# Performance work log

Measured on AMD Instinct MI355X. Metric: run time of the kernel, lower is better.

## Reference

```python
import jax, jax.numpy as jnp
import numpy as np

B = 8
SEQ = 8192
D_MODEL = 256
D_STATE = 64
D_CONV = 4
EXPAND = 4
HEADDIM = 64
N_LAYERS = 8
D_INNER = EXPAND * D_MODEL            # 1024
NHEADS = D_INNER // HEADDIM           # 16
CONV_DIM = D_INNER + 2 * D_STATE      # 1152 (ngroups=1)
D_IN_PROJ = 2 * D_INNER + 2 * D_STATE + NHEADS  # 2192


def setup_inputs():
    key = jax.random.key(0)
    ks = jax.random.split(key, 16)
    rn = lambda k, shape, fan: jax.random.normal(k, shape, jnp.float32) / np.float32(np.sqrt(fan))
    inp = {}
    inp["x"] = jax.random.normal(ks[0], (B, 3, SEQ), jnp.float32)
    inp["conv1_w"] = rn(ks[1], (64, 3, 16), 3 * 16)
    inp["conv1_b"] = rn(ks[2], (64,), 64)
    inp["conv2_w"] = rn(ks[3], (D_MODEL, 64, 16), 64 * 16)
    inp["conv2_b"] = rn(ks[4], (D_MODEL,), D_MODEL)
    inp["in_proj_w"] = rn(ks[5], (N_LAYERS, D_IN_PROJ, D_MODEL), D_MODEL)
    inp["dw_conv_w"] = rn(ks[6], (N_LAYERS, CONV_DIM, D_CONV), D_CONV)
    inp["dw_conv_b"] = rn(ks[7], (N_LAYERS, CONV_DIM), D_CONV)
    inp["dt_bias"] = jax.random.normal(ks[8], (N_LAYERS, NHEADS), jnp.float32) * 0.5
    inp["A_log"] = jax.random.uniform(ks[9], (N_LAYERS, NHEADS), jnp.float32, 0.0, 2.0)
    inp["ssm_D"] = jnp.ones((N_LAYERS, NHEADS), jnp.float32)
    inp["rms_w"] = jnp.ones((N_LAYERS, D_INNER), jnp.float32)
    inp["out_proj_w"] = rn(ks[10], (N_LAYERS, D_MODEL, D_INNER), D_INNER)
    inp["ln_w"] = jnp.ones((D_MODEL,), jnp.float32)
    inp["ln_b"] = jnp.zeros((D_MODEL,), jnp.float32)
    inp["reg1_w"] = rn(ks[11], (128, D_MODEL), D_MODEL)
    inp["reg1_b"] = rn(ks[12], (128,), 128)
    inp["reg2_w"] = rn(ks[13], (1, 128), 128)
    inp["reg2_b"] = rn(ks[14], (1,), 128)
    return inp


def _silu(v):
    return v * jax.nn.sigmoid(v)


def _mamba2_layer(u, in_proj_w, dw_w, dw_b, dt_bias, A_log, ssm_D, rms_w, out_proj_w):
    b, l, _ = u.shape
    zxbcdt = u @ in_proj_w.T                               # (b,l,2192)
    z = zxbcdt[..., :D_INNER]
    xBC = zxbcdt[..., D_INNER:D_INNER + CONV_DIM]
    dt = jax.nn.softplus(zxbcdt[..., D_INNER + CONV_DIM:] + dt_bias)   # (b,l,h)
    # causal depthwise conv1d (kernel D_CONV), then SiLU
    pad = jnp.pad(xBC, ((0, 0), (D_CONV - 1, 0), (0, 0)))
    conv = sum(pad[:, k:k + l, :] * dw_w[:, k] for k in range(D_CONV)) + dw_b
    xBC = _silu(conv)
    xh = xBC[..., :D_INNER].reshape(b, l, NHEADS, HEADDIM)  # (b,l,h,p)
    Bm = xBC[..., D_INNER:D_INNER + D_STATE]                # (b,l,n)
    Cm = xBC[..., D_INNER + D_STATE:]                       # (b,l,n)
    dA = jnp.exp(dt * (-jnp.exp(A_log)))                    # (b,l,h)

    def step(h, inp):
        dA_t, dt_t, x_t, B_t, C_t = inp
        h = h * dA_t[:, :, None, None] + (dt_t[:, :, None] * x_t)[..., None] * B_t[:, None, None, :]
        y = jnp.einsum('bhpn,bn->bhp', h, C_t)
        return h, y

    h0 = jnp.zeros((b, NHEADS, HEADDIM, D_STATE), u.dtype)
    xs = (dA.transpose(1, 0, 2), dt.transpose(1, 0, 2),
          xh.transpose(1, 0, 2, 3), Bm.transpose(1, 0, 2), Cm.transpose(1, 0, 2))
    _, ys = jax.lax.scan(step, h0, xs)                      # (l,b,h,p)
    y = ys.transpose(1, 0, 2, 3) + ssm_D[None, None, :, None] * xh
    y = y.reshape(b, l, D_INNER)
    y = y * _silu(z)                                        # gated
    y = y * jax.lax.rsqrt(jnp.mean(y * y, axis=-1, keepdims=True) + 1e-5) * rms_w
    return y @ out_proj_w.T


def reference(x, conv1_w, conv1_b, conv2_w, conv2_b, in_proj_w, dw_conv_w, dw_conv_b,
              dt_bias, A_log, ssm_D, rms_w, out_proj_w, ln_w, ln_b,
              reg1_w, reg1_b, reg2_w, reg2_b):
    dn = ('NCH', 'OIH', 'NCH')
    h = jax.lax.conv_general_dilated(x, conv1_w, (4,), [(6, 6)], dimension_numbers=dn) + conv1_b[None, :, None]
    h = jax.nn.gelu(h, approximate=False)
    h = jax.lax.conv_general_dilated(h, conv2_w, (2,), [(7, 7)], dimension_numbers=dn) + conv2_b[None, :, None]
    h = jax.nn.gelu(h, approximate=False)
    h = h.transpose(0, 2, 1)                                # (b, 1024, d_model)
    for i in range(N_LAYERS):
        h = _mamba2_layer(h, in_proj_w[i], dw_conv_w[i], dw_conv_b[i],
                          dt_bias[i], A_log[i], ssm_D[i], rms_w[i], out_proj_w[i])
    mu = jnp.mean(h, -1, keepdims=True)
    var = jnp.mean((h - mu) ** 2, -1, keepdims=True)
    h = (h - mu) * jax.lax.rsqrt(var + 1e-5) * ln_w + ln_b  # LayerNorm
    pooled = h.mean(1)
    r = jax.nn.gelu(pooled @ reg1_w.T + reg1_b, approximate=False)
    return r @ reg2_w.T + reg2_b                            # (b, 1)
```

## Files before the change

kernel.cpp:

```cpp
#include <hip/hip_runtime.h>
#include <math.h>

#define NB       8
#define SEQ      8192
#define L1OUT    2048
#define LOUT     1024
#define DMODEL   256
#define DINNER   1024
#define NHEADS   16
#define HEADDIM  64
#define DSTATE   64
#define CONVDIM  1152
#define DINPROJ  2192
#define NPADIN   2304
#define NLAYERS  8
#define NCHUNK   16
#define Q        64

typedef _Float16 f16;
typedef __attribute__((ext_vector_type(8))) _Float16 f16x8;
typedef __attribute__((ext_vector_type(4))) _Float16 f16x4;
typedef __attribute__((ext_vector_type(4))) float    f32x4;

__device__ __forceinline__ float gelu_f(float v) {
    return 0.5f * v * (1.0f + erff(v * 0.70710678118654752f));
}
__device__ __forceinline__ float silu_f(float v) {
    return v * __builtin_amdgcn_rcpf(1.0f + __expf(-v));
}

__device__ __forceinline__ void gload16(const void* g, void* l) {
    __builtin_amdgcn_global_load_lds(
        (const __attribute__((address_space(1))) unsigned int*)g,
        (__attribute__((address_space(3))) unsigned int*)l, 16, 0, 0);
}

__global__ __launch_bounds__(256) void k_cast(const float* __restrict__ in,
                                              f16* __restrict__ out, int n) {
    int i = blockIdx.x * 256 + threadIdx.x;
    if (i < n) out[i] = (f16)in[i];
}

__global__ __launch_bounds__(256) void k_cast_inproj(const float* __restrict__ w,
                                                     f16* __restrict__ out) {
    int idx = blockIdx.x * 256 + threadIdx.x;
    int c = idx & 255;
    int r = (idx >> 8) % NPADIN;
    int l = idx / (NPADIN * 256);
    float v = (r < DINPROJ) ? w[((size_t)l * DINPROJ + r) * 256 + c] : 0.f;
    out[idx] = (f16)v;
}

__global__ __launch_bounds__(256) void k_conv1(const float* __restrict__ x,
                                               const float* __restrict__ w,
                                               const float* __restrict__ bias,
                                               f16* __restrict__ out) {
    int idx = blockIdx.x * 256 + threadIdx.x;
    int u  = idx & 255;
    int co = (idx >> 8) & 63;
    int b  = idx >> 14;
    int xbase = u * 32 - 8;

    float acc[8];
#pragma unroll
    for (int t = 0; t < 8; ++t) acc[t] = bias[co];

#pragma unroll
    for (int ci = 0; ci < 3; ++ci) {
        const float* xp = x + ((size_t)b * 3 + ci) * SEQ;
        float xb[48];
#pragma unroll
        for (int j = 0; j < 12; ++j) {
            int off = xbase + j * 4;
            float4 v;
            if (off >= 0 && off + 3 < SEQ) {
                v = *(const float4*)&xp[off];
            } else {
                v.x = (off + 0 >= 0 && off + 0 < SEQ) ? xp[off + 0] : 0.f;
                v.y = (off + 1 >= 0 && off + 1 < SEQ) ? xp[off + 1] : 0.f;
                v.z = (off + 2 >= 0 && off + 2 < SEQ) ? xp[off + 2] : 0.f;
                v.w = (off + 3 >= 0 && off + 3 < SEQ) ? xp[off + 3] : 0.f;
            }
            xb[j * 4 + 0] = v.x; xb[j * 4 + 1] = v.y;
            xb[j * 4 + 2] = v.z; xb[j * 4 + 3] = v.w;
        }
        const float* wp = w + (co * 3 + ci) * 16;
        float wv[16];
#pragma unroll
        for (int k = 0; k < 16; ++k) wv[k] = wp[k];
#pragma unroll
        for (int t = 0; t < 8; ++t)
#pragma unroll
            for (int k = 0; k < 16; ++k)
                acc[t] = fmaf(xb[t * 4 + k + 2], wv[k], acc[t]);
    }
    f16x8 o;
#pragma unroll
    for (int t = 0; t < 8; ++t) o[t] = (f16)gelu_f(acc[t]);
    *(f16x8*)&out[((size_t)(b * 64 + co)) * L1OUT + u * 8] = o;
}

__global__ __launch_bounds__(256) void k_im2col(const f16* __restrict__ h1,
                                                f16* __restrict__ A) {
    int idx = blockIdx.x * 256 + threadIdx.x;
    int g = idx & 127;
    int row = idx >> 7;
    int t = row & (LOUT - 1);
    int b = row >> 10;
    int ci = g >> 1, k0 = (g & 1) * 8;
    int pos0 = t * 2 + k0 - 7;
    const f16* hp = h1 + ((size_t)(b * 64 + ci)) * L1OUT;
    f16x8 v;
#pragma unroll
    for (int j = 0; j < 8; ++j) {
        int p = pos0 + j;
        v[j] = (p >= 0 && p < L1OUT) ? hp[p] : (f16)0.f;
    }
    *(f16x8*)&A[(size_t)row * 1024 + g * 8] = v;
}

template<int BM, int EPI>
__global__ __launch_bounds__(256) void k_hgemm(const f16* __restrict__ A,
                                               const f16* __restrict__ Bw,
                                               f16* __restrict__ Ch,
                                               int M, int N, int K,
                                               const float* __restrict__ bias,
                                               const float* __restrict__ dt_bias,
                                               const float* __restrict__ A_log,
                                               float* __restrict__ dadt) {
    constexpr int MI = BM / 32;
    __shared__ f16 As[BM * 64];
    __shared__ f16 Bs[128 * 64];
    int tid  = threadIdx.x;
    int lane = tid & 63, wid = tid >> 6;
    int wm = wid >> 1, wn = wid & 1;
    int row0 = blockIdx.y * BM, col0 = blockIdx.x * 128;
    int lr = lane & 15, kb = lane >> 4;

    f32x4 acc[MI][4];
#pragma unroll
    for (int mi = 0; mi < MI; ++mi)
#pragma unroll
        for (int ni = 0; ni < 4; ++ni)
            acc[mi][ni] = (f32x4){0.f, 0.f, 0.f, 0.f};

    int sr  = tid >> 3;
    int scx = ((tid & 7) ^ (sr & 7)) * 8;
    int rsw = (lr & 7) * 8;

    for (int k0 = 0; k0 < K; k0 += 64) {
        __syncthreads();
#pragma unroll
        for (int is = 0; is < BM / 32; ++is)
            gload16(A + (size_t)(row0 + is * 32 + sr) * K + k0 + scx,
                    &As[is * 2048 + wid * 512]);
#pragma unroll
        for (int is = 0; is < 4; ++is)
            gload16(Bw + (size_t)(col0 + is * 32 + sr) * K + k0 + scx,
                    &Bs[is * 2048 + wid * 512]);
        __syncthreads();

#pragma unroll
        for (int ks = 0; ks < 2; ++ks) {
            int cbase = (ks * 32 + kb * 8) ^ rsw;
            f16x8 a[MI], b[4];
#pragma unroll
            for (int mi = 0; mi < MI; ++mi)
                a[mi] = *reinterpret_cast<const f16x8*>(
                    &As[(wm * (BM / 2) + mi * 16 + lr) * 64 + cbase]);
#pragma unroll
            for (int ni = 0; ni < 4; ++ni)
                b[ni] = *reinterpret_cast<const f16x8*>(
                    &Bs[(wn * 64 + ni * 16 + lr) * 64 + cbase]);
#pragma unroll
            for (int mi = 0; mi < MI; ++mi)
#pragma unroll
                for (int ni = 0; ni < 4; ++ni)
                    acc[mi][ni] = __builtin_amdgcn_mfma_f32_16x16x32_f16(
                        a[mi], b[ni], acc[mi][ni], 0, 0, 0);
        }
    }

#pragma unroll
    for (int mi = 0; mi < MI; ++mi)
#pragma unroll
        for (int ni = 0; ni < 4; ++ni) {
            int ccol = col0 + wn * 64 + ni * 16 + lr;
            if (ccol < N) {
                int rbase = row0 + wm * (BM / 2) + mi * 16 + kb * 4;
                f32x4 v = acc[mi][ni];
#pragma unroll
                for (int r = 0; r < 4; ++r) {
                    float val = v[r];
                    if (EPI == 1) val = gelu_f(val + bias[ccol]);
                    Ch[(size_t)(rbase + r) * N + ccol] = (f16)val;
                    if (EPI == 2 && ccol >= DINNER + CONVDIM) {
                        int hh = ccol - (DINNER + CONVDIM);
                        float raw = val + dt_bias[hh];
                        float dtv = (raw > 20.f) ? raw : log1pf(__expf(raw));
                        float lda = -__expf(A_log[hh]) * dtv;
                        *(float2*)&dadt[(size_t)(rbase + r) * 32 + hh * 2] =
                            make_float2(lda, dtv);
                    }
                }
            }
        }
}

__global__ __launch_bounds__(256) void k_ssd1(const f16* __restrict__ zx16,
                                              const float* __restrict__ dadt,
                                              const float* __restrict__ dw_w,
                                              const float* __restrict__ dw_b,
                                              const float* __restrict__ ssmD,
                                              f16* __restrict__ y1,
                                              f16* __restrict__ Sbuf16,
                                              float* __restrict__ Abuf,
                                              f16* __restrict__ C16) {
    __shared__ f16 Bs[64][72];
    __shared__ f16 Cs[64][72];
    __shared__ float GT[64][68];
    __shared__ f16 Mw[4][64][72];
    __shared__ float2 LaDt[4][64];

    int tid = threadIdx.x, lane = tid & 63, wid = tid >> 6;
    int bid = blockIdx.x;
    int hq = bid & 3, c = (bid >> 2) & 15, b = bid >> 6;
    int h = hq * 4 + wid;
    int lr = lane & 15, kb = lane >> 4;
    f16* Xs = &Mw[0][0][0];

    {
        int sg = tid % 48;
        int ts = tid / 48;
        if (ts < 4) {
            int xc;
            if (sg < 32)      xc = hq * 256 + sg * 8;
            else if (sg < 40) xc = 1024 + (sg - 32) * 8;
            else              xc = 1088 + (sg - 40) * 8;
            int zc = 1024 + xc;
            float4 wv[8];
            float  bv[8];
#pragma unroll
            for (int j = 0; j < 8; ++j) {
                wv[j] = *(const float4*)&dw_w[(xc + j) * 4];
                bv[j] = dw_b[xc + j];
            }
            int l0 = c * 64 + ts * 16;
            const f16* zrow = zx16 + ((size_t)(b * 1024 + l0)) * DINPROJ + zc;
            f16x8 r0, r1, r2, r3;
            f16x8 zz;
#pragma unroll
            for (int j = 0; j < 8; ++j) zz[j] = (f16)0.f;
            r0 = (l0 >= 3) ? *(const f16x8*)(zrow - 3 * DINPROJ) : zz;
            r1 = (l0 >= 2) ? *(const f16x8*)(zrow - 2 * DINPROJ) : zz;
            r2 = (l0 >= 1) ? *(const f16x8*)(zrow - 1 * DINPROJ) : zz;
#pragma unroll
            for (int t = 0; t < 16; ++t) {
                r3 = *(const f16x8*)(zrow + t * DINPROJ);
                f16x8 o;
#pragma unroll
                for (int j = 0; j < 8; ++j) {
                    float s = bv[j];
                    s = fmaf((float)r0[j], wv[j].x, s);
                    s = fmaf((float)r1[j], wv[j].y, s);
                    s = fmaf((float)r2[j], wv[j].z, s);
                    s = fmaf((float)r3[j], wv[j].w, s);
                    o[j] = (f16)silu_f(s);
                }
                int row = ts * 16 + t;
                if (sg < 32) {
                    f16x4 o0 = {o[0], o[1], o[2], o[3]};
                    f16x4 o1 = {o[4], o[5], o[6], o[7]};
                    *(f16x4*)&Xs[row * 260 + sg * 8]     = o0;
                    *(f16x4*)&Xs[row * 260 + sg * 8 + 4] = o1;
                } else if (sg < 40) {
                    *(f16x8*)&Bs[row][(sg - 32) * 8] = o;
                } else {
                    *(f16x8*)&Cs[row][(sg - 40) * 8] = o;
                }
                r0 = r1; r1 = r2; r2 = r3;
            }
        }
    }

    float2 ad = *(const float2*)&dadt[((size_t)(b * 1024 + c * 64 + lane) * 16 + h) * 2];
    float La = ad.x;
#pragma unroll
    for (int o = 1; o < 64; o <<= 1) {
        float v = __shfl_up(La, o);
        if (lane >= o) La += v;
    }
    float dt_own = ad.y;
    float La63 = __shfl(La, 63);
    float w_own = __expf(La63 - La) * dt_own;
    LaDt[wid][lane] = make_float2(La, dt_own);
    float Dh = ssmD[h];
    __syncthreads();

    if (hq == 0) {
        f16* cp = C16 + (((size_t)(b * 16 + c)) << 12);
#pragma unroll
        for (int it = 0; it < 2; ++it) {
            int cid = it * 256 + tid;
            int row = cid >> 3, off = (cid & 7) * 8;
            *(f16x8*)&cp[row * 64 + off] = *(const f16x8*)&Cs[row][off];
        }
    }

    f16x8 xfrag[4][2];
#pragma unroll
    for (int pi = 0; pi < 4; ++pi)
#pragma unroll
        for (int ks = 0; ks < 2; ++ks) {
            f16x8 v;
#pragma unroll
            for (int j = 0; j < 8; ++j)
                v[j] = Xs[(ks * 32 + kb * 8 + j) * 260 + wid * 64 + pi * 16 + lr];
            xfrag[pi][ks] = v;
        }

    {
        int tq = wid & 1, sq = wid >> 1;
        f32x4 g[2][2];
#pragma unroll
        for (int i = 0; i < 2; ++i)
#pragma unroll
            for (int j = 0; j < 2; ++j) g[i][j] = (f32x4){0.f, 0.f, 0.f, 0.f};
#pragma unroll
        for (int ks = 0; ks < 2; ++ks) {
            f16x8 a[2], bb[2];
#pragma unroll
            for (int ti = 0; ti < 2; ++ti)
                a[ti] = *(const f16x8*)&Cs[tq * 32 + ti * 16 + lr][ks * 32 + kb * 8];
#pragma unroll
            for (int si = 0; si < 2; ++si)
                bb[si] = *(const f16x8*)&Bs[sq * 32 + si * 16 + lr][ks * 32 + kb * 8];
#pragma unroll
            for (int ti = 0; ti < 2; ++ti)
#pragma unroll
                for (int si = 0; si < 2; ++si)
                    g[ti][si] = __builtin_amdgcn_mfma_f32_16x16x32_f16(
                        a[ti], bb[si], g[ti][si], 0, 0, 0);
        }
#pragma unroll
        for (int ti = 0; ti < 2; ++ti)
#pragma unroll
            for (int si = 0; si < 2; ++si)
#pragma unroll
                for (int r = 0; r < 4; ++r)
                    GT[sq * 32 + si * 16 + lr][tq * 32 + ti * 16 + kb * 4 + r] = g[ti][si][r];
    }
    __syncthreads();

    {
        f16x8 brow[8];
#pragma unroll
        for (int i = 0; i < 8; ++i) brow[i] = *(const f16x8*)&Bs[lane][i * 8];
#pragma unroll
        for (int i = 0; i < 8; ++i)
#pragma unroll
            for (int j = 0; j < 8; ++j)
                Mw[wid][i * 8 + j][lane] = (f16)((float)brow[i][j] * w_own);
    }
    __builtin_amdgcn_wave_barrier();

    f16x8 sbfrag[4][2];
#pragma unroll
    for (int ni = 0; ni < 4; ++ni)
#pragma unroll
        for (int ks = 0; ks < 2; ++ks)
            sbfrag[ni][ks] = *(const f16x8*)&Mw[wid][ni * 16 + lr][ks * 32 + kb * 8];

    {
        f32x4 accS[4][4];
#pragma unroll
        for (int pi = 0; pi < 4; ++pi)
#pragma unroll
            for (int ni = 0; ni < 4; ++ni) accS[pi][ni] = (f32x4){0.f, 0.f, 0.f, 0.f};
#pragma unroll
        for (int ks = 0; ks < 2; ++ks)
#pragma unroll
            for (int pi = 0; pi < 4; ++pi)
#pragma unroll
                for (int ni = 0; ni < 4; ++ni)
                    accS[pi][ni] = __builtin_amdgcn_mfma_f32_16x16x32_f16(
                        xfrag[pi][ks], sbfrag[ni][ks], accS[pi][ni], 0, 0, 0);
        size_t sbase = ((size_t)((b * 16 + h) * 16 + c)) << 12;
#pragma unroll
        for (int pi = 0; pi < 4; ++pi)
#pragma unroll
            for (int ni = 0; ni < 4; ++ni)
#pragma unroll
                for (int r = 0; r < 4; ++r)
                    Sbuf16[sbase + (size_t)(pi * 16 + kb * 4 + r) * 64 + ni * 16 + lr] =
                        (f16)accS[pi][ni][r];
        if (lane == 0) Abuf[(b * 16 + h) * 16 + c] = __expf(La63);
    }
    __builtin_amdgcn_wave_barrier();

    {
        int t = lane;
        float la_t = La;
#pragma unroll
        for (int s8 = 0; s8 < 8; ++s8) {
            f16x8 mv;
#pragma unroll
            for (int j = 0; j < 8; ++j) {
                int s = s8 * 8 + j;
                float2 ld = LaDt[wid][s];
                float m = (s <= t) ? GT[s][t] * __expf(la_t - ld.x) * ld.y : 0.f;
                if (s == t) m += Dh;
                mv[j] = (f16)m;
            }
            *(f16x8*)&Mw[wid][t][s8 * 8] = mv;
        }
    }
    __builtin_amdgcn_wave_barrier();

    {
        f32x4 accY[4][4];
#pragma unroll
        for (int ti = 0; ti < 4; ++ti)
#pragma unroll
            for (int pi = 0; pi < 4; ++pi) accY[ti][pi] = (f32x4){0.f, 0.f, 0.f, 0.f};
#pragma unroll
        for (int ks = 0; ks < 2; ++ks) {
            f16x8 af[4];
#pragma unroll
            for (int ti = 0; ti < 4; ++ti)
                af[ti] = *(const f16x8*)&Mw[wid][ti * 16 + lr][ks * 32 + kb * 8];
#pragma unroll
            for (int ti = 0; ti < 4; ++ti)
#pragma unroll
                for (int pi = 0; pi < 4; ++pi)
                    accY[ti][pi] = __builtin_amdgcn_mfma_f32_16x16x32_f16(
                        af[ti], xfrag[pi][ks], accY[ti][pi], 0, 0, 0);
        }
        f16* yp = y1 + ((size_t)(b * 1024 + c * 64)) * 1024 + h * 64;
#pragma unroll
        for (int ti = 0; ti < 4; ++ti)
#pragma unroll
            for (int pi = 0; pi < 4; ++pi)
#pragma unroll
                for (int r = 0; r < 4; ++r)
                    yp[(size_t)(ti * 16 + kb * 4 + r) * 1024 + pi * 16 + lr] =
                        (f16)accY[ti][pi][r];
    }
}

__global__ __launch_bounds__(256) void k_ssd2f(const f16* __restrict__ C16,
                                               const f16* __restrict__ Sbuf16,
                                               const float* __restrict__ Abuf,
                                               const float* __restrict__ dadt,
                                               f16* __restrict__ y2) {
    __shared__ f16 Hs[NCHUNK][4096];
    int tid = threadIdx.x, lane = tid & 63, wv = tid >> 6;
    int bh = blockIdx.x;
    int h = bh & 15, b = bh >> 4;
    int lr = lane & 15, kb = lane >> 4;
    size_t base = (size_t)bh << 16;

    {
        int off = tid * 16;
        int row = tid >> 2;
        int c0f = (tid & 3) * 16;
        int sw = (row & 7) * 8;
        int d0 = row * 64 + (c0f ^ sw);
        int d1 = row * 64 + ((c0f + 8) ^ sw);
        float Hl[16];
#pragma unroll
        for (int j = 0; j < 16; ++j) Hl[j] = 0.f;
#pragma unroll
        for (int c = 0; c < NCHUNK; ++c) {
            f16x8 o0, o1;
#pragma unroll
            for (int j = 0; j < 8; ++j) { o0[j] = (f16)Hl[j]; o1[j] = (f16)Hl[j + 8]; }
            *(f16x8*)&Hs[c][d0] = o0;
            *(f16x8*)&Hs[c][d1] = o1;
            float A = Abuf[bh * 16 + c];
            f16x8 s0 = *(const f16x8*)&Sbuf16[base + (size_t)c * 4096 + off];
            f16x8 s1 = *(const f16x8*)&Sbuf16[base + (size_t)c * 4096 + off + 8];
#pragma unroll
            for (int j = 0; j < 8; ++j) {
                Hl[j]     = fmaf(Hl[j],     A, (float)s0[j]);
                Hl[j + 8] = fmaf(Hl[j + 8], A, (float)s1[j]);
            }
        }
    }
    __syncthreads();

    const f16* cpb = C16 + ((size_t)b << 16);
#pragma unroll
    for (int i = 0; i < 4; ++i) {
        int c = wv * 4 + i;
        float2 ad = *(const float2*)&dadt[((size_t)(b * 1024 + c * 64 + lane) * 16 + h) * 2];
        float La = ad.x;
#pragma unroll
        for (int o = 1; o < 64; o <<= 1) {
            float v = __shfl_up(La, o);
            if (lane >= o) La += v;
        }

        f16x8 hfrag[4][2];
#pragma unroll
        for (int pi = 0; pi < 4; ++pi)
#pragma unroll
            for (int ks = 0; ks < 2; ++ks) {
                int row = pi * 16 + lr;
                int cf = (ks * 32 + kb * 8) ^ ((row & 7) * 8);
                hfrag[pi][ks] = *(const f16x8*)&Hs[c][row * 64 + cf];
            }

        const f16* cp = cpb + ((size_t)c << 12);
        f32x4 acc[4][4];
#pragma unroll
        for (int ti = 0; ti < 4; ++ti)
#pragma unroll
            for (int pi = 0; pi < 4; ++pi) acc[ti][pi] = (f32x4){0.f, 0.f, 0.f, 0.f};
#pragma unroll
        for (int ks = 0; ks < 2; ++ks) {
            f16x8 af[4];
#pragma unroll
            for (int ti = 0; ti < 4; ++ti)
                af[ti] = *(const f16x8*)(cp + (ti * 16 + lr) * 64 + ks * 32 + kb * 8);
#pragma unroll
            for (int ti = 0; ti < 4; ++ti)
#pragma unroll
                for (int pi = 0; pi < 4; ++pi)
                    acc[ti][pi] = __builtin_amdgcn_mfma_f32_16x16x32_f16(
                        af[ti], hfrag[pi][ks], acc[ti][pi], 0, 0, 0);
        }
        f16* yp = y2 + ((size_t)(b * 1024 + c * 64)) * 1024 + h * 64;
#pragma unroll
        for (int ti = 0; ti < 4; ++ti)
#pragma unroll
            for (int r = 0; r < 4; ++r) {
                int t = ti * 16 + kb * 4 + r;
                float sc = __expf(__shfl(La, t));
#pragma unroll
                for (int pi = 0; pi < 4; ++pi)
                    yp[(size_t)t * 1024 + pi * 16 + lr] = (f16)(sc * acc[ti][pi][r]);
            }
    }
}

__global__ __launch_bounds__(256) void k_gate(const f16* __restrict__ zx16,
                                              const float* __restrict__ rmsw,
                                              const f16* __restrict__ y1,
                                              const f16* __restrict__ y2,
                                              f16* __restrict__ ygate) {
    __shared__ float sh[4];
    int bl = blockIdx.x, tid = threadIdx.x;
    int c = tid * 4;
    f16x4 y1v = *reinterpret_cast<const f16x4*>(&y1[(size_t)bl * DINNER + c]);
    f16x4 y2v = *reinterpret_cast<const f16x4*>(&y2[(size_t)bl * DINNER + c]);
    f16x4 z4  = *reinterpret_cast<const f16x4*>(&zx16[(size_t)bl * DINPROJ + c]);
    float v[4];
    float ss = 0.f;
#pragma unroll
    for (int j = 0; j < 4; ++j) {
        v[j] = ((float)y1v[j] + (float)y2v[j]) * silu_f((float)z4[j]);
        ss += v[j] * v[j];
    }
    int lane = tid & 63, wid = tid >> 6;
#pragma unroll
    for (int o = 32; o > 0; o >>= 1) ss += __shfl_down(ss, o, 64);
    if (lane == 0) sh[wid] = ss;
    __syncthreads();
    float total = sh[0] + sh[1] + sh[2] + sh[3];
    float r = rsqrtf(total * (1.f / DINNER) + 1e-5f);
    f16x4 o4;
    o4.x = (f16)(v[0] * r * rmsw[c + 0]);
    o4.y = (f16)(v[1] * r * rmsw[c + 1]);
    o4.z = (f16)(v[2] * r * rmsw[c + 2]);
    o4.w = (f16)(v[3] * r * rmsw[c + 3]);
    *reinterpret_cast<f16x4*>(&ygate[(size_t)bl * DINNER + c]) = o4;
}

__global__ __launch_bounds__(256) void k_lnpool(const f16* __restrict__ h,
                                                const float* __restrict__ lnw,
                                                const float* __restrict__ lnb,
                                                float* __restrict__ pooledp) {
    __shared__ float pl[4][256];
    int bid = blockIdx.x;
    int b = bid >> 5, seg = bid & 31;
    int tid = threadIdx.x, lane = tid & 63, w = tid >> 6;
    int c4 = lane * 4;
    float4 lw = *(const float4*)&lnw[c4];
    float4 lb = *(const float4*)&lnb[c4];
    float acc0 = 0.f, acc1 = 0.f, acc2 = 0.f, acc3 = 0.f;
    const f16* hb = h + ((size_t)b * 1024 + seg * 32 + w * 8) * DMODEL;
#pragma unroll
    for (int i = 0; i < 8; ++i) {
        f16x4 hv = *(const f16x4*)(hb + (size_t)i * DMODEL + c4);
        float vx = (float)hv.x, vy = (float)hv.y, vz = (float)hv.z, vw = (float)hv.w;
        float s1 = vx + vy + vz + vw;
        float s2 = vx * vx + vy * vy + vz * vz + vw * vw;
#pragma unroll
        for (int o = 32; o > 0; o >>= 1) {
            s1 += __shfl_xor(s1, o);
            s2 += __shfl_xor(s2, o);
        }
        float mu = s1 * (1.f / DMODEL);
        float var = s2 * (1.f / DMODEL) - mu * mu;
        float rr = rsqrtf(var + 1e-5f);
        acc0 += (vx - mu) * rr * lw.x + lb.x;
        acc1 += (vy - mu) * rr * lw.y + lb.y;
        acc2 += (vz - mu) * rr * lw.z + lb.z;
        acc3 += (vw - mu) * rr * lw.w + lb.w;
    }
    pl[w][c4 + 0] = acc0; pl[w][c4 + 1] = acc1;
    pl[w][c4 + 2] = acc2; pl[w][c4 + 3] = acc3;
    __syncthreads();
    float tot = pl[0][tid] + pl[1][tid] + pl[2][tid] + pl[3][tid];
    pooledp[(size_t)(b * 32 + seg) * 256 + tid] = tot;
}

__global__ __launch_bounds__(128) void k_head(const float* __restrict__ pooledp,
                                              const float* __restrict__ w1,
                                              const float* __restrict__ b1,
                                              const float* __restrict__ w2,
                                              const float* __restrict__ b2,
                                              float* __restrict__ out) {
    __shared__ float sp[256];
    __shared__ float red[2];
    int b = blockIdx.x, j = threadIdx.x;
    for (int d = j; d < 256; d += 128) {
        float s = 0.f;
#pragma unroll
        for (int seg = 0; seg < 32; ++seg)
            s += pooledp[(size_t)(b * 32 + seg) * 256 + d];
        sp[d] = s * (1.f / LOUT);
    }
    __syncthreads();
    float acc = b1[j];
#pragma unroll 8
    for (int d = 0; d < DMODEL; ++d)
        acc = fmaf(sp[d], w1[j * DMODEL + d], acc);
    float r = gelu_f(acc) * w2[j];
#pragma unroll
    for (int o = 32; o > 0; o >>= 1) r += __shfl_down(r, o, 64);
    int lane = j & 63, wid = j >> 6;
    if (lane == 0) red[wid] = r;
    __syncthreads();
    if (j == 0) out[b] = red[0] + red[1] + b2[0];
}

extern "C" void kernel_launch(void* const* d_in, const int* in_sizes, int n_in,
                              void* d_out, int out_size, void* d_ws, size_t ws_size,
                              hipStream_t stream) {
    const float* x         = (const float*)d_in[0];
    const float* conv1_w   = (const float*)d_in[1];
    const float* conv1_b   = (const float*)d_in[2];
    const float* conv2_w   = (const float*)d_in[3];
    const float* conv2_b   = (const float*)d_in[4];
    const float* in_proj_w = (const float*)d_in[5];
    const float* dw_w      = (const float*)d_in[6];
    const float* dw_b      = (const float*)d_in[7];
    const float* dt_bias   = (const float*)d_in[8];
    const float* A_log     = (const float*)d_in[9];
    const float* ssm_D     = (const float*)d_in[10];
    const float* rms_w     = (const float*)d_in[11];
    const float* out_proj_w= (const float*)d_in[12];
    const float* ln_w      = (const float*)d_in[13];
    const float* ln_b      = (const float*)d_in[14];
    const float* reg1_w    = (const float*)d_in[15];
    const float* reg1_b    = (const float*)d_in[16];
    const float* reg2_w    = (const float*)d_in[17];
    const float* reg2_b    = (const float*)d_in[18];

    float* ws = (float*)d_ws;
    size_t off = 0;
    float* dadt    = ws + off; off += (size_t)NB * LOUT * NHEADS * 2;
    float* Abuf    = ws + off; off += (size_t)NB * NHEADS * NCHUNK;
    float* pooledp = ws + off; off += (size_t)NB * 32 * 256;

    f16* fbase = (f16*)(ws + off);
    size_t foff = 0;
    f16* c1f16  = fbase + foff; foff += (size_t)NB * 64 * L1OUT;
    f16* hbf0   = fbase + foff; foff += (size_t)NB * LOUT * DMODEL;
    f16* hbf1   = fbase + foff; foff += (size_t)NB * LOUT * DMODEL;
    f16* ygate  = fbase + foff; foff += (size_t)NB * LOUT * DINNER;
    f16* y2     = fbase + foff; foff += (size_t)NB * LOUT * DINNER;
    f16* y1     = fbase + foff; foff += (size_t)NB * LOUT * DINNER;
    f16* C16    = fbase + foff; foff += (size_t)NB * NCHUNK * 64 * 64;
    f16* zx16   = fbase + foff; foff += (size_t)NB * LOUT * DINPROJ;
    f16* Sbuf16 = fbase + foff; foff += (size_t)NB * NHEADS * NCHUNK * 4096;
    f16* w_in_h = fbase + foff; foff += (size_t)NLAYERS * NPADIN * DMODEL;
    f16* w_out_h= fbase + foff; foff += (size_t)NLAYERS * DMODEL * DINNER;
    f16* w_c2_h = fbase + foff; foff += (size_t)DMODEL * 1024;
    f16* im2h   = y1;

    k_cast_inproj<<<(NLAYERS * NPADIN * 256) / 256, 256, 0, stream>>>(in_proj_w, w_in_h);
    k_cast<<<(NLAYERS * DMODEL * DINNER) / 256, 256, 0, stream>>>(
        out_proj_w, w_out_h, NLAYERS * DMODEL * DINNER);
    k_cast<<<(DMODEL * 1024) / 256, 256, 0, stream>>>(conv2_w, w_c2_h, DMODEL * 1024);

    k_conv1<<<(NB * 64 * 256) / 256, 256, 0, stream>>>(x, conv1_w, conv1_b, c1f16);
    k_im2col<<<(NB * LOUT * 128) / 256, 256, 0, stream>>>(c1f16, im2h);
    {
        dim3 g(256 / 128, 8192 / 64);
        k_hgemm<64, 1><<<g, 256, 0, stream>>>(im2h, w_c2_h, hbf0,
                                              8192, 256, 1024, conv2_b,
                                              nullptr, nullptr, nullptr);
    }

    f16* hcur = hbf0;
    f16* hnxt = hbf1;
    for (int i = 0; i < NLAYERS; ++i) {
        {
            dim3 g(NPADIN / 128, 8192 / 128);
            k_hgemm<128, 2><<<g, 256, 0, stream>>>(
                hcur, w_in_h + (size_t)i * NPADIN * DMODEL, zx16,
                8192, DINPROJ, DMODEL, nullptr,
                dt_bias + i * NHEADS, A_log + i * NHEADS, dadt);
        }
        k_ssd1<<<NB * NCHUNK * 4, 256, 0, stream>>>(
            zx16, dadt, dw_w + (size_t)i * CONVDIM * 4, dw_b + (size_t)i * CONVDIM,
            ssm_D + i * NHEADS, y1, Sbuf16, Abuf, C16);
        k_ssd2f<<<NB * NHEADS, 256, 0, stream>>>(C16, Sbuf16, Abuf, dadt, y2);
        k_gate<<<NB * LOUT, 256, 0, stream>>>(zx16, rms_w + (size_t)i * DINNER,
                                              y1, y2, ygate);
        {
            dim3 g(DMODEL / 128, 8192 / 64);
            k_hgemm<64, 0><<<g, 256, 0, stream>>>(
                ygate, w_out_h + (size_t)i * DMODEL * DINNER, hnxt,
                8192, DMODEL, DINNER, nullptr, nullptr, nullptr, nullptr);
        }
        f16* tmp = hcur; hcur = hnxt; hnxt = tmp;
    }

    k_lnpool<<<NB * 32, 256, 0, stream>>>(hcur, ln_w, ln_b, pooledp);
    k_head<<<NB, 128, 0, stream>>>(pooledp, reg1_w, reg1_b, reg2_w, reg2_b, (float*)d_out);
}
```

Baseline: 875.9 us.

## Fuse gating and RMSNorm into out-projection GEMM, fold rms weight into weights

Replaces the separate gate/RMSNorm kernel and the out-projection GEMM with one kernel. It computes the gated rows for a 32-row tile into LDS, finds the per-row RMS scale, runs MFMA against the out-projection weights, and applies the scale in the epilogue. The RMS weight is folded into the fp16 out-projection weights during a single merged cast kernel that replaces three cast launches. This removes the ygate round trip through global memory and a launch per layer. In exchange it uses a 64 KB LDS A-tile and only 256 blocks, each reloading the full weight matrix, which may limit occupancy and GEMM efficiency.

```diff
diff --git a/kernel.cpp b/kernel.cpp
--- a/kernel.cpp
+++ b/kernel.cpp
@@ -17,6 +17,10 @@
 #define NCHUNK   16
 #define Q        64
 
+#define N_CAST1 (NLAYERS * NPADIN * DMODEL)
+#define N_CAST2 (NLAYERS * DMODEL * DINNER)
+#define N_CAST3 (DMODEL * 1024)
+
 typedef _Float16 f16;
 typedef __attribute__((ext_vector_type(8))) _Float16 f16x8;
 typedef __attribute__((ext_vector_type(4))) _Float16 f16x4;
@@ -35,20 +39,29 @@
         (__attribute__((address_space(3))) unsigned int*)l, 16, 0, 0);
 }
 
-__global__ __launch_bounds__(256) void k_cast(const float* __restrict__ in,
-                                              f16* __restrict__ out, int n) {
-    int i = blockIdx.x * 256 + threadIdx.x;
-    if (i < n) out[i] = (f16)in[i];
-}
-
-__global__ __launch_bounds__(256) void k_cast_inproj(const float* __restrict__ w,
-                                                     f16* __restrict__ out) {
+__global__ __launch_bounds__(256) void k_castall(const float* __restrict__ w_in,
+                                                 const float* __restrict__ w_out,
+                                                 const float* __restrict__ rmsw,
+                                                 const float* __restrict__ w_c2,
+                                                 f16* __restrict__ o_in,
+                                                 f16* __restrict__ o_out,
+                                                 f16* __restrict__ o_c2) {
     int idx = blockIdx.x * 256 + threadIdx.x;
-    int c = idx & 255;
-    int r = (idx >> 8) % NPADIN;
-    int l = idx / (NPADIN * 256);
-    float v = (r < DINPROJ) ? w[((size_t)l * DINPROJ + r) * 256 + c] : 0.f;
-    out[idx] = (f16)v;
+    if (idx < N_CAST1) {
+        int c = idx & 255;
+        int r = (idx >> 8) % NPADIN;
+        int l = idx / (NPADIN * 256);
+        float v = (r < DINPROJ) ? w_in[((size_t)l * DINPROJ + r) * 256 + c] : 0.f;
+        o_in[idx] = (f16)v;
+    } else if (idx < N_CAST1 + N_CAST2) {
+        int i = idx - N_CAST1;
+        int k = i % DINNER;
+        int l = i / (DMODEL * DINNER);
+        o_out[i] = (f16)(w_out[i] * rmsw[l * DINNER + k]);
+    } else if (idx < N_CAST1 + N_CAST2 + N_CAST3) {
+        int i = idx - N_CAST1 - N_CAST2;
+        o_c2[i] = (f16)w_c2[i];
+    }
 }
 
 __global__ __launch_bounds__(256) void k_conv1(const float* __restrict__ x,
@@ -544,37 +557,86 @@
     }
 }
 
-__global__ __launch_bounds__(256) void k_gate(const f16* __restrict__ zx16,
-                                              const float* __restrict__ rmsw,
-                                              const f16* __restrict__ y1,
-                                              const f16* __restrict__ y2,
-                                              f16* __restrict__ ygate) {
-    __shared__ float sh[4];
-    int bl = blockIdx.x, tid = threadIdx.x;
-    int c = tid * 4;
-    f16x4 y1v = *reinterpret_cast<const f16x4*>(&y1[(size_t)bl * DINNER + c]);
-    f16x4 y2v = *reinterpret_cast<const f16x4*>(&y2[(size_t)bl * DINNER + c]);
-    f16x4 z4  = *reinterpret_cast<const f16x4*>(&zx16[(size_t)bl * DINPROJ + c]);
-    float v[4];
-    float ss = 0.f;
-#pragma unroll
-    for (int j = 0; j < 4; ++j) {
-        v[j] = ((float)y1v[j] + (float)y2v[j]) * silu_f((float)z4[j]);
-        ss += v[j] * v[j];
-    }
-    int lane = tid & 63, wid = tid >> 6;
-#pragma unroll
-    for (int o = 32; o > 0; o >>= 1) ss += __shfl_down(ss, o, 64);
-    if (lane == 0) sh[wid] = ss;
-    __syncthreads();
-    float total = sh[0] + sh[1] + sh[2] + sh[3];
-    float r = rsqrtf(total * (1.f / DINNER) + 1e-5f);
-    f16x4 o4;
-    o4.x = (f16)(v[0] * r * rmsw[c + 0]);
-    o4.y = (f16)(v[1] * r * rmsw[c + 1]);
-    o4.z = (f16)(v[2] * r * rmsw[c + 2]);
-    o4.w = (f16)(v[3] * r * rmsw[c + 3]);
-    *reinterpret_cast<f16x4*>(&ygate[(size_t)bl * DINNER + c]) = o4;
+__global__ __launch_bounds__(512) void k_oproj(const f16* __restrict__ y1,
+                                               const f16* __restrict__ y2,
+                                               const f16* __restrict__ zx16,
+                                               const f16* __restrict__ Bw,
+                                               f16* __restrict__ out) {
+    __shared__ f16 As[32 * 1024];
+    __shared__ f16 Bs[128 * 64];
+    __shared__ float Rs[32];
+    int tid = threadIdx.x, lane = tid & 63, wid = tid >> 6;
+    int row0 = blockIdx.x * 32;
+    int lr = lane & 15, kb = lane >> 4;
+
+    {
+        int row = tid >> 4, seg = tid & 15;
+        const f16* p1 = y1 + (size_t)(row0 + row) * DINNER + seg * 64;
+        const f16* p2 = y2 + (size_t)(row0 + row) * DINNER + seg * 64;
+        const f16* pz = zx16 + (size_t)(row0 + row) * DINPROJ + seg * 64;
+        float ss = 0.f;
+#pragma unroll
+        for (int i = 0; i < 8; ++i) {
+            f16x8 a = *(const f16x8*)(p1 + i * 8);
+            f16x8 bb = *(const f16x8*)(p2 + i * 8);
+            f16x8 z = *(const f16x8*)(pz + i * 8);
+            f16x8 o;
+#pragma unroll
+            for (int j = 0; j < 8; ++j) {
+                float v = ((float)a[j] + (float)bb[j]) * silu_f((float)z[j]);
+                ss += v * v;
+                o[j] = (f16)v;
+            }
+            int c8 = seg * 8 + i;
+            *(f16x8*)&As[row * 1024 + (c8 ^ (row & 7)) * 8] = o;
+        }
+        ss += __shfl_xor(ss, 1); ss += __shfl_xor(ss, 2);
+        ss += __shfl_xor(ss, 4); ss += __shfl_xor(ss, 8);
+        if (seg == 0) Rs[row] = rsqrtf(ss * (1.f / DINNER) + 1e-5f);
+    }
+
+    int wm = wid >> 2, wn = wid & 3;
+    int sr = tid >> 3;
+    int scx = ((tid & 7) ^ (sr & 7)) * 8;
+    int rsw = (lr & 7) * 8;
+
+    for (int nh = 0; nh < 2; ++nh) {
+        f32x4 acc[2];
+#pragma unroll
+        for (int ni = 0; ni < 2; ++ni) acc[ni] = (f32x4){0.f, 0.f, 0.f, 0.f};
+
+        for (int k0 = 0; k0 < DINNER; k0 += 64) {
+            __syncthreads();
+#pragma unroll
+            for (int is = 0; is < 2; ++is)
+                gload16(Bw + (size_t)(nh * 128 + is * 64 + sr) * DINNER + k0 + scx,
+                        &Bs[is * 4096 + wid * 512]);
+            __syncthreads();
+
+#pragma unroll
+            for (int ks = 0; ks < 2; ++ks) {
+                int cbase = (ks * 32 + kb * 8) ^ rsw;
+                f16x8 a = *reinterpret_cast<const f16x8*>(
+                    &As[(wm * 16 + lr) * 1024 + k0 + cbase]);
+                f16x8 b0 = *reinterpret_cast<const f16x8*>(
+                    &Bs[(wn * 32 + lr) * 64 + cbase]);
+                f16x8 b1 = *reinterpret_cast<const f16x8*>(
+                    &Bs[(wn * 32 + 16 + lr) * 64 + cbase]);
+                acc[0] = __builtin_amdgcn_mfma_f32_16x16x32_f16(a, b0, acc[0], 0, 0, 0);
+                acc[1] = __builtin_amdgcn_mfma_f32_16x16x32_f16(a, b1, acc[1], 0, 0, 0);
+            }
+        }
+#pragma unroll
+        for (int ni = 0; ni < 2; ++ni) {
+            int ccol = nh * 128 + wn * 32 + ni * 16 + lr;
+#pragma unroll
+            for (int r = 0; r < 4; ++r) {
+                int orow = wm * 16 + kb * 4 + r;
+                out[(size_t)(row0 + orow) * DMODEL + ccol] =
+                    (f16)(acc[ni][r] * Rs[orow]);
+            }
+        }
+    }
 }
 
 __global__ __launch_bounds__(256) void k_lnpool(const f16* __restrict__ h,
@@ -680,7 +742,6 @@
     f16* c1f16  = fbase + foff; foff += (size_t)NB * 64 * L1OUT;
     f16* hbf0   = fbase + foff; foff += (size_t)NB * LOUT * DMODEL;
     f16* hbf1   = fbase + foff; foff += (size_t)NB * LOUT * DMODEL;
-    f16* ygate  = fbase + foff; foff += (size_t)NB * LOUT * DINNER;
     f16* y2     = fbase + foff; foff += (size_t)NB * LOUT * DINNER;
     f16* y1     = fbase + foff; foff += (size_t)NB * LOUT * DINNER;
     f16* C16    = fbase + foff; foff += (size_t)NB * NCHUNK * 64 * 64;
@@ -691,10 +752,11 @@
     f16* w_c2_h = fbase + foff; foff += (size_t)DMODEL * 1024;
     f16* im2h   = y1;
 
-    k_cast_inproj<<<(NLAYERS * NPADIN * 256) / 256, 256, 0, stream>>>(in_proj_w, w_in_h);
-    k_cast<<<(NLAYERS * DMODEL * DINNER) / 256, 256, 0, stream>>>(
-        out_proj_w, w_out_h, NLAYERS * DMODEL * DINNER);
-    k_cast<<<(DMODEL * 1024) / 256, 256, 0, stream>>>(conv2_w, w_c2_h, DMODEL * 1024);
+    {
+        int total = N_CAST1 + N_CAST2 + N_CAST3;
+        k_castall<<<(total + 255) / 256, 256, 0, stream>>>(
+            in_proj_w, out_proj_w, rms_w, conv2_w, w_in_h, w_out_h, w_c2_h);
+    }
 
     k_conv1<<<(NB * 64 * 256) / 256, 256, 0, stream>>>(x, conv1_w, conv1_b, c1f16);
     k_im2col<<<(NB * LOUT * 128) / 256, 256, 0, stream>>>(c1f16, im2h);
@@ -719,14 +781,8 @@
             zx16, dadt, dw_w + (size_t)i * CONVDIM * 4, dw_b + (size_t)i * CONVDIM,
             ssm_D + i * NHEADS, y1, Sbuf16, Abuf, C16);
         k_ssd2f<<<NB * NHEADS, 256, 0, stream>>>(C16, Sbuf16, Abuf, dadt, y2);
-        k_gate<<<NB * LOUT, 256, 0, stream>>>(zx16, rms_w + (size_t)i * DINNER,
-                                              y1, y2, ygate);
-        {
-            dim3 g(DMODEL / 128, 8192 / 64);
-            k_hgemm<64, 0><<<g, 256, 0, stream>>>(
-                ygate, w_out_h + (size_t)i * DMODEL * DINNER, hnxt,
-                8192, DMODEL, DINNER, nullptr, nullptr, nullptr, nullptr);
-        }
+        k_oproj<<<8192 / 32, 512, 0, stream>>>(
+            y1, y2, zx16, w_out_h + (size_t)i * DMODEL * DINNER, hnxt);
         f16* tmp = hcur; hcur = hnxt; hnxt = tmp;
     }
 
```

Result: slower. 1.005 ms (+14.8%).

## Remap blocks across XCDs for L2 locality and merge weight cast kernels

Applied to the files above, without the earlier changes.

Adds an XCD-aware block index remapping so consecutive logical tiles land on the same XCD, applied to the GEMM, ssd1 and ssd2f kernels. The aim is to improve L2 reuse of shared A/B tiles and chunk data on MI355X's multi-die layout. It also fuses the three weight cast kernels into one launch to cut launch overhead. The remap assumes the block count is divisible by 8, and the GEMM grids and the ssd kernels satisfy this.

```diff
diff --git a/kernel.cpp b/kernel.cpp
--- a/kernel.cpp
+++ b/kernel.cpp
@@ -17,6 +17,10 @@
 #define NCHUNK   16
 #define Q        64
 
+#define N_CAST1 (NLAYERS * NPADIN * DMODEL)
+#define N_CAST2 (NLAYERS * DMODEL * DINNER)
+#define N_CAST3 (DMODEL * 1024)
+
 typedef _Float16 f16;
 typedef __attribute__((ext_vector_type(8))) _Float16 f16x8;
 typedef __attribute__((ext_vector_type(4))) _Float16 f16x4;
@@ -35,20 +39,30 @@
         (__attribute__((address_space(3))) unsigned int*)l, 16, 0, 0);
 }
 
-__global__ __launch_bounds__(256) void k_cast(const float* __restrict__ in,
-                                              f16* __restrict__ out, int n) {
-    int i = blockIdx.x * 256 + threadIdx.x;
-    if (i < n) out[i] = (f16)in[i];
-}
-
-__global__ __launch_bounds__(256) void k_cast_inproj(const float* __restrict__ w,
-                                                     f16* __restrict__ out) {
+__device__ __forceinline__ int xcd_chunk(int flat, int nblk) {
+    return (flat & 7) * (nblk >> 3) + (flat >> 3);
+}
+
+__global__ __launch_bounds__(256) void k_castall(const float* __restrict__ w_in,
+                                                 const float* __restrict__ w_out,
+                                                 const float* __restrict__ w_c2,
+                                                 f16* __restrict__ o_in,
+                                                 f16* __restrict__ o_out,
+                                                 f16* __restrict__ o_c2) {
     int idx = blockIdx.x * 256 + threadIdx.x;
-    int c = idx & 255;
-    int r = (idx >> 8) % NPADIN;
-    int l = idx / (NPADIN * 256);
-    float v = (r < DINPROJ) ? w[((size_t)l * DINPROJ + r) * 256 + c] : 0.f;
-    out[idx] = (f16)v;
+    if (idx < N_CAST1) {
+        int c = idx & 255;
+        int r = (idx >> 8) % NPADIN;
+        int l = idx / (NPADIN * 256);
+        float v = (r < DINPROJ) ? w_in[((size_t)l * DINPROJ + r) * 256 + c] : 0.f;
+        o_in[idx] = (f16)v;
+    } else if (idx < N_CAST1 + N_CAST2) {
+        int i = idx - N_CAST1;
+        o_out[i] = (f16)w_out[i];
+    } else if (idx < N_CAST1 + N_CAST2 + N_CAST3) {
+        int i = idx - N_CAST1 - N_CAST2;
+        o_c2[i] = (f16)w_c2[i];
+    }
 }
 
 __global__ __launch_bounds__(256) void k_conv1(const float* __restrict__ x,
@@ -134,7 +148,11 @@
     int tid  = threadIdx.x;
     int lane = tid & 63, wid = tid >> 6;
     int wm = wid >> 1, wn = wid & 1;
-    int row0 = blockIdx.y * BM, col0 = blockIdx.x * 128;
+
+    int nbx = gridDim.x;
+    int flat = blockIdx.y * nbx + blockIdx.x;
+    int logical = xcd_chunk(flat, nbx * gridDim.y);
+    int row0 = (logical / nbx) * BM, col0 = (logical % nbx) * 128;
     int lr = lane & 15, kb = lane >> 4;
 
     f32x4 acc[MI][4];
@@ -223,7 +241,7 @@
     __shared__ float2 LaDt[4][64];
 
     int tid = threadIdx.x, lane = tid & 63, wid = tid >> 6;
-    int bid = blockIdx.x;
+    int bid = xcd_chunk(blockIdx.x, NB * NCHUNK * 4);
     int hq = bid & 3, c = (bid >> 2) & 15, b = bid >> 6;
     int h = hq * 4 + wid;
     int lr = lane & 15, kb = lane >> 4;
@@ -455,7 +473,7 @@
                                                f16* __restrict__ y2) {
     __shared__ f16 Hs[NCHUNK][4096];
     int tid = threadIdx.x, lane = tid & 63, wv = tid >> 6;
-    int bh = blockIdx.x;
+    int bh = xcd_chunk(blockIdx.x, NB * NHEADS);
     int h = bh & 15, b = bh >> 4;
     int lr = lane & 15, kb = lane >> 4;
     size_t base = (size_t)bh << 16;
@@ -691,10 +709,11 @@
     f16* w_c2_h = fbase + foff; foff += (size_t)DMODEL * 1024;
     f16* im2h   = y1;
 
-    k_cast_inproj<<<(NLAYERS * NPADIN * 256) / 256, 256, 0, stream>>>(in_proj_w, w_in_h);
-    k_cast<<<(NLAYERS * DMODEL * DINNER) / 256, 256, 0, stream>>>(
-        out_proj_w, w_out_h, NLAYERS * DMODEL * DINNER);
-    k_cast<<<(DMODEL * 1024) / 256, 256, 0, stream>>>(conv2_w, w_c2_h, DMODEL * 1024);
+    {
+        int total = N_CAST1 + N_CAST2 + N_CAST3;
+        k_castall<<<(total + 255) / 256, 256, 0, stream>>>(
+            in_proj_w, out_proj_w, conv2_w, w_in_h, w_out_h, w_c2_h);
+    }
 
     k_conv1<<<(NB * 64 * 256) / 256, 256, 0, stream>>>(x, conv1_w, conv1_b, c1f16);
     k_im2col<<<(NB * LOUT * 128) / 256, 256, 0, stream>>>(c1f16, im2h);
```

Result: faster. 849.4 us (-3.0%).
